# Performance work log

Hardware: AMD Instinct MI355X
Metric: run time of the kernel (lower is better)

Reference implementation:

```python
import jax, jax.numpy as jnp
import numpy as np

L_LAYERS = 2
N = 128
T = 64
K_BANDS = 30
KMOD = K_BANDS + 2  # 32
B = 4
G4 = 4 * N
EPS = 1e-5


def setup_inputs() -> dict:
    key = jax.random.key(0)
    ks = iter(jax.random.split(key, 32))
    s = 1.0 / np.sqrt(N)

    def u(shape):
        return jax.random.uniform(next(ks), shape, jnp.float32, -s, s)

    inp = {"x": jax.random.normal(next(ks), (B, KMOD, T, N), jnp.float32)}
    # temporal modules: KMOD LSTM/fc instances per layer
    inp["tw_ih"] = u((L_LAYERS, KMOD, 2, G4, N))
    inp["tw_hh"] = u((L_LAYERS, KMOD, 2, G4, N))
    inp["tb_ih"] = u((L_LAYERS, KMOD, 2, G4))
    inp["tb_hh"] = u((L_LAYERS, KMOD, 2, G4))
    inp["tfc_w"] = u((L_LAYERS, KMOD, N, 2 * N))
    inp["tfc_b"] = u((L_LAYERS, KMOD, N))
    inp["tgn_g"] = jnp.ones((L_LAYERS, N), jnp.float32)
    inp["tgn_b"] = jnp.zeros((L_LAYERS, N), jnp.float32)
    # band modules: T LSTM/fc instances per layer
    inp["bw_ih"] = u((L_LAYERS, T, 2, G4, N))
    inp["bw_hh"] = u((L_LAYERS, T, 2, G4, N))
    inp["bb_ih"] = u((L_LAYERS, T, 2, G4))
    inp["bb_hh"] = u((L_LAYERS, T, 2, G4))
    inp["bfc_w"] = u((L_LAYERS, T, N, 2 * N))
    inp["bfc_b"] = u((L_LAYERS, T, N))
    inp["bgn_g"] = jnp.ones((L_LAYERS, N), jnp.float32)
    inp["bgn_b"] = jnp.zeros((L_LAYERS, N), jnp.float32)
    return inp


def groupnorm(X, gamma, beta):
    # GroupNorm(1, N) on [B, N, K, T] == normalize over all non-batch dims,
    # per-channel affine on the last (N) dim of the [B, K, T, N] layout.
    mu = X.mean(axis=(1, 2, 3), keepdims=True)
    var = X.var(axis=(1, 2, 3), keepdims=True)
    return (X - mu) * jax.lax.rsqrt(var + EPS) * gamma + beta


def bilstm(x, w_ih, w_hh, b_ih, b_hh):
    # x: [B, S, N]; w_ih/w_hh: [2, 4N, N]; biases: [2, 4N]. PyTorch gate order i,f,g,o.
    Bb, S, n = x.shape

    def run(xs, wih, whh, b):
        pre = jnp.einsum('bsn,gn->bsg', xs, wih) + b  # [B, S, 4N]

        def step(carry, p):
            h, c = carry
            g = p + h @ whh.T
            i, f, gg, o = jnp.split(g, 4, axis=-1)
            c = jax.nn.sigmoid(f) * c + jax.nn.sigmoid(i) * jnp.tanh(gg)
            h = jax.nn.sigmoid(o) * jnp.tanh(c)
            return (h, c), h

        z = jnp.zeros((Bb, n), xs.dtype)
        _, hs = jax.lax.scan(step, (z, z), jnp.swapaxes(pre, 0, 1))
        return jnp.swapaxes(hs, 0, 1)  # [B, S, N]

    fwd = run(x, w_ih[0], w_hh[0], b_ih[0] + b_hh[0])
    bwd = run(x[:, ::-1], w_ih[1], w_hh[1], b_ih[1] + b_hh[1])[:, ::-1]
    return jnp.concatenate([fwd, bwd], axis=-1)  # [B, S, 2N]


# vmap over the per-instance (band or frame) leading axis of inputs and weights
vbilstm = jax.vmap(bilstm, in_axes=(0, 0, 0, 0, 0))


def temporal_module(X, w_ih, w_hh, b_ih, b_hh, fc_w, fc_b, g, b):
    skip = X  # [B, K, T, N]
    Xn = groupnorm(X, g, b)
    xs = jnp.swapaxes(Xn, 0, 1)  # [K, B, T, N]
    h = vbilstm(xs, w_ih, w_hh, b_ih, b_hh)  # [K, B, T, 2N]
    out = jnp.einsum('kbtd,knd->kbtn', h, fc_w) + fc_b[:, None, None, :]
    return jnp.swapaxes(out, 0, 1) + skip


def band_module(X, w_ih, w_hh, b_ih, b_hh, fc_w, fc_b, g, b):
    skip = X  # [B, K, T, N]
    Xn = groupnorm(X, g, b)
    xs = jnp.transpose(Xn, (2, 0, 1, 3))  # [T, B, K, N]
    h = vbilstm(xs, w_ih, w_hh, b_ih, b_hh)  # [T, B, K, 2N]
    out = jnp.einsum('tbkd,tnd->tbkn', h, fc_w) + fc_b[:, None, None, :]
    return jnp.transpose(out, (1, 2, 0, 3)) + skip


def reference(x, tw_ih, tw_hh, tb_ih, tb_hh, tfc_w, tfc_b, tgn_g, tgn_b,
              bw_ih, bw_hh, bb_ih, bb_hh, bfc_w, bfc_b, bgn_g, bgn_b):
    X = x
    for i in range(L_LAYERS):
        X = temporal_module(X, tw_ih[i], tw_hh[i], tb_ih[i], tb_hh[i],
                            tfc_w[i], tfc_b[i], tgn_g[i], tgn_b[i])
        X = band_module(X, bw_ih[i], bw_hh[i], bb_ih[i], bb_hh[i],
                        bfc_w[i], bfc_b[i], bgn_g[i], bgn_b[i])
    return X[:, :K_BANDS, :, :]
```

## Files before the change

### kernel.cpp

```cpp
#include <hip/hip_runtime.h>
#include <hip/hip_bf16.h>
#include <cstddef>

#define BB 4
#define KK 32
#define TTT 64
#define NNC 128
#define GG4 512

__global__ void k_copy(const float4* __restrict__ src, float4* __restrict__ dst, int n4) {
    int i = blockIdx.x * blockDim.x + threadIdx.x;
    if (i < n4) dst[i] = src[i];
}

__global__ void k_gnred(const float* __restrict__ X, float* __restrict__ red) {
    int b = blockIdx.x >> 6, chunk = blockIdx.x & 63;
    const float4* p4 = (const float4*)(X + (size_t)b * 262144 + (size_t)chunk * 4096);
    float s = 0.f, ss = 0.f;
#pragma unroll
    for (int i = 0; i < 4; ++i) {
        float4 v = p4[threadIdx.x + i * 256];
        s  += v.x + v.y + v.z + v.w;
        ss += v.x * v.x + v.y * v.y + v.z * v.z + v.w * v.w;
    }
    for (int off = 32; off; off >>= 1) {
        s  += __shfl_down(s, off);
        ss += __shfl_down(ss, off);
    }
    __shared__ float l0[4], l1[4];
    int w = threadIdx.x >> 6;
    if ((threadIdx.x & 63) == 0) { l0[w] = s; l1[w] = ss; }
    __syncthreads();
    if (threadIdx.x == 0) {
        float a = l0[0] + l0[1] + l0[2] + l0[3];
        float c = l1[0] + l1[1] + l1[2] + l1[3];
        red[(b * 64 + chunk) * 2]     = a;
        red[(b * 64 + chunk) * 2 + 1] = c;
    }
}

__device__ __forceinline__ float sigm(float x) { return 1.f / (1.f + __expf(-x)); }
__device__ __forceinline__ float tanh_fast(float x) {
    x = fminf(fmaxf(x, -15.f), 15.f);
    float e = __expf(2.f * x);
    return (e - 1.f) / (e + 1.f);
}

template <bool BAND>
__global__ __launch_bounds__(1024, 1) void k_pre(
    const float* __restrict__ X, float* __restrict__ pre,
    const float* __restrict__ red,
    const float* __restrict__ w_ih,
    const float* __restrict__ b_ih, const float* __restrict__ b_hh,
    const float* __restrict__ gn_g, const float* __restrict__ gn_b,
    int layer)
{
    constexpr int S    = BAND ? 32 : 64;
    constexpr int INST = BAND ? 64 : 32;
    const int tid = threadIdx.x;
    const int g   = tid & 511;
    const int hh  = tid >> 9;
    const int bid = blockIdx.x;
    const int b = bid & 3, dir = (bid >> 2) & 1, inst = bid >> 3;

    __shared__ float xn[S * 128];
    __shared__ float ex[4][1024];
    __shared__ float biasl[512];

    float s0 = 0.f, s1 = 0.f;
    {
        const float* rp = red + b * 128;
#pragma unroll 16
        for (int i = 0; i < 128; i += 2) { s0 += rp[i]; s1 += rp[i + 1]; }
    }
    const float mu = s0 * (1.0f / 262144.0f);
    const float rs = rsqrtf(fmaxf(s1 * (1.0f / 262144.0f) - mu * mu, 0.f) + 1e-5f);

    const size_t wbase = ((size_t)layer * INST + inst) * 2 + dir;
    if (tid < 512) biasl[tid] = b_ih[wbase * 512 + tid] + b_hh[wbase * 512 + tid];

    {
        const size_t xbase = BAND ? ((size_t)b * 2048 + inst) * 128
                                  : ((size_t)b * 32 + inst) * 64 * 128;
        const float* gmg = gn_g + layer * 128;
        const float* gmb = gn_b + layer * 128;
        for (int i4 = tid; i4 < S * 32; i4 += 1024) {
            int srow = i4 >> 5, n4 = i4 & 31;
            const float4 v = *(const float4*)(X + xbase +
                              (BAND ? (size_t)srow * 8192 : (size_t)srow * 128) + n4 * 4);
            const float4 ga = *(const float4*)(gmg + n4 * 4);
            const float4 be = *(const float4*)(gmb + n4 * 4);
            float4 o;
            o.x = (v.x - mu) * rs * ga.x + be.x;
            o.y = (v.y - mu) * rs * ga.y + be.y;
            o.z = (v.z - mu) * rs * ga.z + be.z;
            o.w = (v.w - mu) * rs * ga.w + be.w;
            *(float4*)(xn + srow * 128 + n4 * 4) = o;
        }
    }

    float4 w4[16];
    {
        const float* wr = w_ih + (wbase * 512 + g) * 128 + hh * 64;
#pragma unroll
        for (int j = 0; j < 16; ++j) w4[j] = *(const float4*)(wr + 4 * j);
    }
    __syncthreads();

    float* pb = pre + (size_t)bid * (S * 512);
    for (int st0 = 0; st0 < S; st0 += 4) {
#pragma unroll
        for (int q = 0; q < 4; ++q) {
            const int st = st0 + q;
            const int sidx = dir ? (S - 1 - st) : st;
            const float* xr = xn + sidx * 128 + hh * 64;
            float acc = 0.f;
#pragma unroll
            for (int j = 0; j < 16; ++j) {
                float4 hv = *(const float4*)(xr + 4 * j);
                acc += w4[j].x * hv.x + w4[j].y * hv.y + w4[j].z * hv.z + w4[j].w * hv.w;
            }
            ex[q][hh * 512 + g] = acc;
        }
        __syncthreads();
        for (int idx = tid; idx < 4 * 512; idx += 1024) {
            int q = idx >> 9, gg = idx & 511;
            pb[(size_t)(st0 + q) * 512 + gg] = ex[q][gg] + ex[q][512 + gg] + biasl[gg];
        }
        __syncthreads();
    }
}

template <bool BAND>
__global__ __launch_bounds__(1024, 1) void k_scan2(
    const float* __restrict__ pre, float* __restrict__ hout,
    const float* __restrict__ w_hh, int layer)
{
    constexpr int S    = BAND ? 32 : 64;
    constexpr int INST = BAND ? 64 : 32;
    constexpr int CH   = 8;
    const int tid = threadIdx.x;
    const int g   = tid & 511;
    const int hh  = tid >> 9;
    const int bid = blockIdx.x;
    const int b = bid & 3, dir = (bid >> 2) & 1, inst = bid >> 3;

    __shared__ float plds[2][CH * 512];
    __shared__ float ex[1024];
    __shared__ float hbuf[128];

    const size_t wbase = ((size_t)layer * INST + inst) * 2 + dir;
    float4 w4[16];
    {
        const float* wr = w_hh + (wbase * 512 + g) * 128 + hh * 64;
#pragma unroll
        for (int j = 0; j < 16; ++j) w4[j] = *(const float4*)(wr + 4 * j);
    }

    const float* pb = pre + (size_t)bid * (S * 512);
    ((float4*)plds[0])[tid] = ((const float4*)pb)[tid];
    if (tid < 128) hbuf[tid] = 0.f;
    float c = 0.f;
    float4 pf = make_float4(0.f, 0.f, 0.f, 0.f);
    __syncthreads();

    float* hob = hout + ((size_t)inst * 4 + b) * S * 256 + dir * 128;

    for (int ch = 0; ch < S / CH; ++ch) {
        const int buf = ch & 1;
        if (ch + 1 < S / CH)
            pf = ((const float4*)(pb + (size_t)(ch + 1) * CH * 512))[tid];
#pragma unroll
        for (int q = 0; q < CH; ++q) {
            const float* hr = hbuf + hh * 64;
            float acc = (hh == 0) ? plds[buf][q * 512 + g] : 0.f;
#pragma unroll
            for (int j = 0; j < 16; ++j) {
                float4 hv = *(const float4*)(hr + 4 * j);
                acc += w4[j].x * hv.x + w4[j].y * hv.y + w4[j].z * hv.z + w4[j].w * hv.w;
            }
            ex[hh * 512 + g] = acc;
            __syncthreads();
            if (tid < 128) {
                const float gi = ex[tid]       + ex[512 + tid];
                const float gf = ex[128 + tid] + ex[640 + tid];
                const float gg = ex[256 + tid] + ex[768 + tid];
                const float go = ex[384 + tid] + ex[896 + tid];
                c = sigm(gf) * c + sigm(gi) * tanh_fast(gg);
                const float hv = sigm(go) * tanh_fast(c);
                hbuf[tid] = hv;
                const int st = ch * CH + q;
                const int sidx = dir ? (S - 1 - st) : st;
                hob[(size_t)sidx * 256 + tid] = hv;
            }
            __syncthreads();
        }
        if (ch + 1 < S / CH) {
            ((float4*)plds[buf ^ 1])[tid] = pf;
            __syncthreads();
        }
    }
}

template <bool BAND>
__global__ void k_fc(const float* __restrict__ h, const float* __restrict__ fc_w,
                     const float* __restrict__ fc_b, float* __restrict__ X, int layer)
{
    constexpr int S    = BAND ? 32 : 64;
    constexpr int INST = BAND ? 64 : 32;
    constexpr int RPB  = 8;
    const int inst  = blockIdx.x / (BB * S / RPB);
    const int chunk = blockIdx.x % (BB * S / RPB);

    __shared__ float hs[RPB * 256];
    const int tid = threadIdx.x;
    const float* hbase = h + ((size_t)inst * BB * S + chunk * RPB) * 256;
    for (int i = tid; i < RPB * 64; i += 256)
        ((float4*)hs)[i] = ((const float4*)hbase)[i];
    __syncthreads();

    const int n  = tid & 127;
    const int rg = tid >> 7;
    const float* wrow = fc_w + (((size_t)layer * INST + inst) * 128 + n) * 256;
    float a0 = 0.f, a1 = 0.f, a2 = 0.f, a3 = 0.f;
#pragma unroll 8
    for (int d4 = 0; d4 < 64; ++d4) {
        float4 wv = ((const float4*)wrow)[d4];
        float4 h0 = ((const float4*)(hs + (rg * 4 + 0) * 256))[d4];
        float4 h1 = ((const float4*)(hs + (rg * 4 + 1) * 256))[d4];
        float4 h2 = ((const float4*)(hs + (rg * 4 + 2) * 256))[d4];
        float4 h3 = ((const float4*)(hs + (rg * 4 + 3) * 256))[d4];
        a0 += wv.x * h0.x + wv.y * h0.y + wv.z * h0.z + wv.w * h0.w;
        a1 += wv.x * h1.x + wv.y * h1.y + wv.z * h1.z + wv.w * h1.w;
        a2 += wv.x * h2.x + wv.y * h2.y + wv.z * h2.z + wv.w * h2.w;
        a3 += wv.x * h3.x + wv.y * h3.y + wv.z * h3.z + wv.w * h3.w;
    }
    const float bias = fc_b[((size_t)layer * INST + inst) * 128 + n];
    float acc[4] = {a0, a1, a2, a3};
#pragma unroll
    for (int i = 0; i < 4; ++i) {
        const int r = chunk * RPB + rg * 4 + i;
        const int b = r / S, s = r % S;
        const size_t xi = BAND ? (((size_t)b * 32 + s) * 64 + inst) * 128 + n
                               : (((size_t)b * 32 + inst) * 64 + s) * 128 + n;
        X[xi] += acc[i] + bias;
    }
}

__global__ void k_slice(const float* __restrict__ X, float* __restrict__ out) {
    int i = blockIdx.x * 256 + threadIdx.x;
    if (i >= 245760) return;
    int n4 = i & 31;
    int r  = i >> 5;
    int t  = r & 63;
    int bk = r >> 6;
    int k  = bk % 30, b = bk / 30;
    ((float4*)out)[i] = *(const float4*)(X + (((size_t)b * 32 + k) * 64 + t) * 128 + (size_t)n4 * 4);
}

extern "C" void kernel_launch(void* const* d_in, const int* in_sizes, int n_in,
                              void* d_out, int out_size, void* d_ws, size_t ws_size,
                              hipStream_t stream) {
    const float* x     = (const float*)d_in[0];
    const float* tw_ih = (const float*)d_in[1];
    const float* tw_hh = (const float*)d_in[2];
    const float* tb_ih = (const float*)d_in[3];
    const float* tb_hh = (const float*)d_in[4];
    const float* tfc_w = (const float*)d_in[5];
    const float* tfc_b = (const float*)d_in[6];
    const float* tgn_g = (const float*)d_in[7];
    const float* tgn_b = (const float*)d_in[8];
    const float* bw_ih = (const float*)d_in[9];
    const float* bw_hh = (const float*)d_in[10];
    const float* bb_ih = (const float*)d_in[11];
    const float* bb_hh = (const float*)d_in[12];
    const float* bfc_w = (const float*)d_in[13];
    const float* bfc_b = (const float*)d_in[14];
    const float* bgn_g = (const float*)d_in[15];
    const float* bgn_b = (const float*)d_in[16];

    float* X   = (float*)d_ws;
    float* h   = X + 1048576;
    float* red = h + 2097152;
    float* pre = red + 512;

    k_copy<<<1024, 256, 0, stream>>>((const float4*)x, (float4*)X, 262144);

    for (int layer = 0; layer < 2; ++layer) {
        k_gnred<<<256, 256, 0, stream>>>(X, red);
        k_pre<false><<<256, 1024, 0, stream>>>(X, pre, red, tw_ih, tb_ih, tb_hh,
                                               tgn_g, tgn_b, layer);
        k_scan2<false><<<256, 1024, 0, stream>>>(pre, h, tw_hh, layer);
        k_fc<false><<<1024, 256, 0, stream>>>(h, tfc_w, tfc_b, X, layer);
        k_gnred<<<256, 256, 0, stream>>>(X, red);
        k_pre<true><<<512, 1024, 0, stream>>>(X, pre, red, bw_ih, bb_ih, bb_hh,
                                              bgn_g, bgn_b, layer);
        k_scan2<true><<<512, 1024, 0, stream>>>(pre, h, bw_hh, layer);
        k_fc<true><<<1024, 256, 0, stream>>>(h, bfc_w, bfc_b, X, layer);
    }

    k_slice<<<960, 256, 0, stream>>>(X, (float*)d_out);
}
```

Before: 943.5 us.

## Fuse groupnorm stats into fc/copy, restructure LSTM scan with shuffle reductions

The standalone groupnorm reduction kernels are removed. Partial sum and sum-of-squares are now computed in the initial copy and in the epilogue of each fc kernel, and the final slice is written directly from the last band fc. The recurrent scan is reorganised so each hidden unit is handled by 8 lanes that own all four gates, reduced with xor shuffles. The pre-activations are stored gate-interleaved, and the h state is double-buffered, so each timestep needs one barrier instead of two. This cuts launches and per-step synchronisation, at the cost of more partial-sum reads in k_pre.

```diff
diff --git a/kernel.cpp b/kernel.cpp
--- a/kernel.cpp
+++ b/kernel.cpp
@@ -8,37 +8,6 @@
 #define NNC 128
 #define GG4 512
 
-__global__ void k_copy(const float4* __restrict__ src, float4* __restrict__ dst, int n4) {
-    int i = blockIdx.x * blockDim.x + threadIdx.x;
-    if (i < n4) dst[i] = src[i];
-}
-
-__global__ void k_gnred(const float* __restrict__ X, float* __restrict__ red) {
-    int b = blockIdx.x >> 6, chunk = blockIdx.x & 63;
-    const float4* p4 = (const float4*)(X + (size_t)b * 262144 + (size_t)chunk * 4096);
-    float s = 0.f, ss = 0.f;
-#pragma unroll
-    for (int i = 0; i < 4; ++i) {
-        float4 v = p4[threadIdx.x + i * 256];
-        s  += v.x + v.y + v.z + v.w;
-        ss += v.x * v.x + v.y * v.y + v.z * v.z + v.w * v.w;
-    }
-    for (int off = 32; off; off >>= 1) {
-        s  += __shfl_down(s, off);
-        ss += __shfl_down(ss, off);
-    }
-    __shared__ float l0[4], l1[4];
-    int w = threadIdx.x >> 6;
-    if ((threadIdx.x & 63) == 0) { l0[w] = s; l1[w] = ss; }
-    __syncthreads();
-    if (threadIdx.x == 0) {
-        float a = l0[0] + l0[1] + l0[2] + l0[3];
-        float c = l1[0] + l1[1] + l1[2] + l1[3];
-        red[(b * 64 + chunk) * 2]     = a;
-        red[(b * 64 + chunk) * 2 + 1] = c;
-    }
-}
-
 __device__ __forceinline__ float sigm(float x) { return 1.f / (1.f + __expf(-x)); }
 __device__ __forceinline__ float tanh_fast(float x) {
     x = fminf(fmaxf(x, -15.f), 15.f);
@@ -46,10 +15,32 @@
     return (e - 1.f) / (e + 1.f);
 }
 
+__global__ void k_copy_red(const float4* __restrict__ src, float4* __restrict__ dst,
+                           float* __restrict__ red2) {
+    const int i = blockIdx.x * 256 + threadIdx.x;
+    const float4 v = src[i];
+    dst[i] = v;
+    float s  = v.x + v.y + v.z + v.w;
+    float ss = v.x * v.x + v.y * v.y + v.z * v.z + v.w * v.w;
+    for (int off = 32; off; off >>= 1) {
+        s  += __shfl_down(s, off);
+        ss += __shfl_down(ss, off);
+    }
+    __shared__ float l0[4], l1[4];
+    const int w = threadIdx.x >> 6;
+    if ((threadIdx.x & 63) == 0) { l0[w] = s; l1[w] = ss; }
+    __syncthreads();
+    if (threadIdx.x == 0) {
+        const int b = blockIdx.x >> 8, slot = blockIdx.x & 255;
+        red2[(b * 256 + slot) * 2]     = l0[0] + l0[1] + l0[2] + l0[3];
+        red2[(b * 256 + slot) * 2 + 1] = l1[0] + l1[1] + l1[2] + l1[3];
+    }
+}
+
 template <bool BAND>
 __global__ __launch_bounds__(1024, 1) void k_pre(
     const float* __restrict__ X, float* __restrict__ pre,
-    const float* __restrict__ red,
+    const float* __restrict__ red2,
     const float* __restrict__ w_ih,
     const float* __restrict__ b_ih, const float* __restrict__ b_hh,
     const float* __restrict__ gn_g, const float* __restrict__ gn_b,
@@ -69,9 +60,9 @@
 
     float s0 = 0.f, s1 = 0.f;
     {
-        const float* rp = red + b * 128;
-#pragma unroll 16
-        for (int i = 0; i < 128; i += 2) { s0 += rp[i]; s1 += rp[i + 1]; }
+        const float* rp = red2 + b * 512;
+#pragma unroll 8
+        for (int i = 0; i < 512; i += 2) { s0 += rp[i]; s1 += rp[i + 1]; }
     }
     const float mu = s0 * (1.0f / 262144.0f);
     const float rs = rsqrtf(fmaxf(s1 * (1.0f / 262144.0f) - mu * mu, 0.f) + 1e-5f);
@@ -114,103 +105,147 @@
             const int st = st0 + q;
             const int sidx = dir ? (S - 1 - st) : st;
             const float* xr = xn + sidx * 128 + hh * 64;
-            float acc = 0.f;
-#pragma unroll
-            for (int j = 0; j < 16; ++j) {
-                float4 hv = *(const float4*)(xr + 4 * j);
-                acc += w4[j].x * hv.x + w4[j].y * hv.y + w4[j].z * hv.z + w4[j].w * hv.w;
+            float a0 = 0.f, a1 = 0.f, a2 = 0.f, a3 = 0.f;
+#pragma unroll
+            for (int j = 0; j < 4; ++j) {
+                float4 hv0 = *(const float4*)(xr + 16 * j);
+                float4 hv1 = *(const float4*)(xr + 16 * j + 4);
+                float4 hv2 = *(const float4*)(xr + 16 * j + 8);
+                float4 hv3 = *(const float4*)(xr + 16 * j + 12);
+                a0 += w4[4*j].x   * hv0.x + w4[4*j].y   * hv0.y + w4[4*j].z   * hv0.z + w4[4*j].w   * hv0.w;
+                a1 += w4[4*j+1].x * hv1.x + w4[4*j+1].y * hv1.y + w4[4*j+1].z * hv1.z + w4[4*j+1].w * hv1.w;
+                a2 += w4[4*j+2].x * hv2.x + w4[4*j+2].y * hv2.y + w4[4*j+2].z * hv2.z + w4[4*j+2].w * hv2.w;
+                a3 += w4[4*j+3].x * hv3.x + w4[4*j+3].y * hv3.y + w4[4*j+3].z * hv3.z + w4[4*j+3].w * hv3.w;
             }
-            ex[q][hh * 512 + g] = acc;
+            ex[q][hh * 512 + g] = (a0 + a1) + (a2 + a3);
         }
         __syncthreads();
         for (int idx = tid; idx < 4 * 512; idx += 1024) {
-            int q = idx >> 9, gg = idx & 511;
-            pb[(size_t)(st0 + q) * 512 + gg] = ex[q][gg] + ex[q][512 + gg] + biasl[gg];
+            const int q = idx >> 9, gg = idx & 511;
+            const int u = gg & 127, gt = gg >> 7;
+            pb[(size_t)(st0 + q) * 512 + u * 4 + gt] =
+                ex[q][gg] + ex[q][512 + gg] + biasl[gg];
         }
         __syncthreads();
     }
 }
 
 template <bool BAND>
-__global__ __launch_bounds__(1024, 1) void k_scan2(
+__global__ __launch_bounds__(1024, 1) void k_scan3(
     const float* __restrict__ pre, float* __restrict__ hout,
     const float* __restrict__ w_hh, int layer)
 {
     constexpr int S    = BAND ? 32 : 64;
     constexpr int INST = BAND ? 64 : 32;
     constexpr int CH   = 8;
+    constexpr int NCH  = S / CH;
     const int tid = threadIdx.x;
-    const int g   = tid & 511;
-    const int hh  = tid >> 9;
+    const int u   = tid >> 3;
+    const int j   = tid & 7;
     const int bid = blockIdx.x;
     const int b = bid & 3, dir = (bid >> 2) & 1, inst = bid >> 3;
 
     __shared__ float plds[2][CH * 512];
-    __shared__ float ex[1024];
-    __shared__ float hbuf[128];
+    __shared__ float hbuf[2][128];
 
     const size_t wbase = ((size_t)layer * INST + inst) * 2 + dir;
-    float4 w4[16];
+    float4 w4[4][4];
     {
-        const float* wr = w_hh + (wbase * 512 + g) * 128 + hh * 64;
-#pragma unroll
-        for (int j = 0; j < 16; ++j) w4[j] = *(const float4*)(wr + 4 * j);
+        const float* wb = w_hh + wbase * 512 * 128;
+#pragma unroll
+        for (int gt = 0; gt < 4; ++gt) {
+            const float* wr = wb + (size_t)(gt * 128 + u) * 128 + j * 16;
+#pragma unroll
+            for (int k = 0; k < 4; ++k) w4[gt][k] = *(const float4*)(wr + 4 * k);
+        }
     }
 
     const float* pb = pre + (size_t)bid * (S * 512);
     ((float4*)plds[0])[tid] = ((const float4*)pb)[tid];
-    if (tid < 128) hbuf[tid] = 0.f;
+    if (tid < 256) ((float*)hbuf)[tid] = 0.f;
+    __syncthreads();
+
     float c = 0.f;
-    float4 pf = make_float4(0.f, 0.f, 0.f, 0.f);
-    __syncthreads();
-
-    float* hob = hout + ((size_t)inst * 4 + b) * S * 256 + dir * 128;
-
-    for (int ch = 0; ch < S / CH; ++ch) {
+    float* hob = hout + (((size_t)inst * 4 + b) * S) * 256 + dir * 128;
+
+    int cur = 0;
+    float4 pf;
+    for (int ch = 0; ch < NCH; ++ch) {
         const int buf = ch & 1;
-        if (ch + 1 < S / CH)
+        if (ch + 1 < NCH)
             pf = ((const float4*)(pb + (size_t)(ch + 1) * CH * 512))[tid];
 #pragma unroll
         for (int q = 0; q < CH; ++q) {
-            const float* hr = hbuf + hh * 64;
-            float acc = (hh == 0) ? plds[buf][q * 512 + g] : 0.f;
-#pragma unroll
-            for (int j = 0; j < 16; ++j) {
-                float4 hv = *(const float4*)(hr + 4 * j);
-                acc += w4[j].x * hv.x + w4[j].y * hv.y + w4[j].z * hv.z + w4[j].w * hv.w;
+            const float* hr = &hbuf[cur][j * 16];
+            const float4 hv0 = *(const float4*)(hr);
+            const float4 hv1 = *(const float4*)(hr + 4);
+            const float4 hv2 = *(const float4*)(hr + 8);
+            const float4 hv3 = *(const float4*)(hr + 12);
+            float acc0, acc1, acc2, acc3;
+            {
+                float a;
+                a  = w4[0][0].x*hv0.x + w4[0][0].y*hv0.y + w4[0][0].z*hv0.z + w4[0][0].w*hv0.w;
+                a += w4[0][1].x*hv1.x + w4[0][1].y*hv1.y + w4[0][1].z*hv1.z + w4[0][1].w*hv1.w;
+                a += w4[0][2].x*hv2.x + w4[0][2].y*hv2.y + w4[0][2].z*hv2.z + w4[0][2].w*hv2.w;
+                a += w4[0][3].x*hv3.x + w4[0][3].y*hv3.y + w4[0][3].z*hv3.z + w4[0][3].w*hv3.w;
+                acc0 = a;
+                a  = w4[1][0].x*hv0.x + w4[1][0].y*hv0.y + w4[1][0].z*hv0.z + w4[1][0].w*hv0.w;
+                a += w4[1][1].x*hv1.x + w4[1][1].y*hv1.y + w4[1][1].z*hv1.z + w4[1][1].w*hv1.w;
+                a += w4[1][2].x*hv2.x + w4[1][2].y*hv2.y + w4[1][2].z*hv2.z + w4[1][2].w*hv2.w;
+                a += w4[1][3].x*hv3.x + w4[1][3].y*hv3.y + w4[1][3].z*hv3.z + w4[1][3].w*hv3.w;
+                acc1 = a;
+                a  = w4[2][0].x*hv0.x + w4[2][0].y*hv0.y + w4[2][0].z*hv0.z + w4[2][0].w*hv0.w;
+                a += w4[2][1].x*hv1.x + w4[2][1].y*hv1.y + w4[2][1].z*hv1.z + w4[2][1].w*hv1.w;
+                a += w4[2][2].x*hv2.x + w4[2][2].y*hv2.y + w4[2][2].z*hv2.z + w4[2][2].w*hv2.w;
+                a += w4[2][3].x*hv3.x + w4[2][3].y*hv3.y + w4[2][3].z*hv3.z + w4[2][3].w*hv3.w;
+                acc2 = a;
+                a  = w4[3][0].x*hv0.x + w4[3][0].y*hv0.y + w4[3][0].z*hv0.z + w4[3][0].w*hv0.w;
+                a += w4[3][1].x*hv1.x + w4[3][1].y*hv1.y + w4[3][1].z*hv1.z + w4[3][1].w*hv1.w;
+                a += w4[3][2].x*hv2.x + w4[3][2].y*hv2.y + w4[3][2].z*hv2.z + w4[3][2].w*hv2.w;
+                a += w4[3][3].x*hv3.x + w4[3][3].y*hv3.y + w4[3][3].z*hv3.z + w4[3][3].w*hv3.w;
+                acc3 = a;
             }
-            ex[hh * 512 + g] = acc;
-            __syncthreads();
-            if (tid < 128) {
-                const float gi = ex[tid]       + ex[512 + tid];
-                const float gf = ex[128 + tid] + ex[640 + tid];
-                const float gg = ex[256 + tid] + ex[768 + tid];
-                const float go = ex[384 + tid] + ex[896 + tid];
-                c = sigm(gf) * c + sigm(gi) * tanh_fast(gg);
-                const float hv = sigm(go) * tanh_fast(c);
-                hbuf[tid] = hv;
+#pragma unroll
+            for (int off = 1; off < 8; off <<= 1) {
+                acc0 += __shfl_xor(acc0, off);
+                acc1 += __shfl_xor(acc1, off);
+                acc2 += __shfl_xor(acc2, off);
+                acc3 += __shfl_xor(acc3, off);
+            }
+            const float4 p4 = *(const float4*)&plds[buf][q * 512 + u * 4];
+            const float gi = acc0 + p4.x;
+            const float gf = acc1 + p4.y;
+            const float gG = acc2 + p4.z;
+            const float go = acc3 + p4.w;
+            c = sigm(gf) * c + sigm(gi) * tanh_fast(gG);
+            const float hval = sigm(go) * tanh_fast(c);
+            const int nxt = cur ^ 1;
+            if (j == 0) {
+                hbuf[nxt][u] = hval;
                 const int st = ch * CH + q;
                 const int sidx = dir ? (S - 1 - st) : st;
-                hob[(size_t)sidx * 256 + tid] = hv;
+                hob[(size_t)sidx * 256 + u] = hval;
             }
+            if (q == CH - 1 && ch + 1 < NCH)
+                ((float4*)plds[buf ^ 1])[tid] = pf;
             __syncthreads();
-        }
-        if (ch + 1 < S / CH) {
-            ((float4*)plds[buf ^ 1])[tid] = pf;
-            __syncthreads();
+            cur = nxt;
         }
     }
 }
 
 template <bool BAND>
 __global__ void k_fc(const float* __restrict__ h, const float* __restrict__ fc_w,
-                     const float* __restrict__ fc_b, float* __restrict__ X, int layer)
+                     const float* __restrict__ fc_b, float* __restrict__ X,
+                     float* __restrict__ red2, float* __restrict__ out,
+                     int layer, int final_out)
 {
     constexpr int S    = BAND ? 32 : 64;
     constexpr int INST = BAND ? 64 : 32;
     constexpr int RPB  = 8;
-    const int inst  = blockIdx.x / (BB * S / RPB);
-    const int chunk = blockIdx.x % (BB * S / RPB);
+    constexpr int CPB  = S / RPB;
+    const int inst  = blockIdx.x / (BB * CPB);
+    const int chunk = blockIdx.x % (BB * CPB);
 
     __shared__ float hs[RPB * 256];
     const int tid = threadIdx.x;
@@ -222,7 +257,7 @@
     const int n  = tid & 127;
     const int rg = tid >> 7;
     const float* wrow = fc_w + (((size_t)layer * INST + inst) * 128 + n) * 256;
-    float a0 = 0.f, a1 = 0.f, a2 = 0.f, a3 = 0.f;
+    float4 a0 = {0,0,0,0}, a1 = {0,0,0,0}, a2 = {0,0,0,0}, a3 = {0,0,0,0};
 #pragma unroll 8
     for (int d4 = 0; d4 < 64; ++d4) {
         float4 wv = ((const float4*)wrow)[d4];
@@ -230,32 +265,45 @@
         float4 h1 = ((const float4*)(hs + (rg * 4 + 1) * 256))[d4];
         float4 h2 = ((const float4*)(hs + (rg * 4 + 2) * 256))[d4];
         float4 h3 = ((const float4*)(hs + (rg * 4 + 3) * 256))[d4];
-        a0 += wv.x * h0.x + wv.y * h0.y + wv.z * h0.z + wv.w * h0.w;
-        a1 += wv.x * h1.x + wv.y * h1.y + wv.z * h1.z + wv.w * h1.w;
-        a2 += wv.x * h2.x + wv.y * h2.y + wv.z * h2.z + wv.w * h2.w;
-        a3 += wv.x * h3.x + wv.y * h3.y + wv.z * h3.z + wv.w * h3.w;
+        a0.x += wv.x*h0.x; a0.y += wv.y*h0.y; a0.z += wv.z*h0.z; a0.w += wv.w*h0.w;
+        a1.x += wv.x*h1.x; a1.y += wv.y*h1.y; a1.z += wv.z*h1.z; a1.w += wv.w*h1.w;
+        a2.x += wv.x*h2.x; a2.y += wv.y*h2.y; a2.z += wv.z*h2.z; a2.w += wv.w*h2.w;
+        a3.x += wv.x*h3.x; a3.y += wv.y*h3.y; a3.z += wv.z*h3.z; a3.w += wv.w*h3.w;
     }
     const float bias = fc_b[((size_t)layer * INST + inst) * 128 + n];
-    float acc[4] = {a0, a1, a2, a3};
+    float acc[4];
+    acc[0] = (a0.x + a0.y) + (a0.z + a0.w);
+    acc[1] = (a1.x + a1.y) + (a1.z + a1.w);
+    acc[2] = (a2.x + a2.y) + (a2.z + a2.w);
+    acc[3] = (a3.x + a3.y) + (a3.z + a3.w);
+
+    float s = 0.f, ss = 0.f;
 #pragma unroll
     for (int i = 0; i < 4; ++i) {
         const int r = chunk * RPB + rg * 4 + i;
-        const int b = r / S, s = r % S;
-        const size_t xi = BAND ? (((size_t)b * 32 + s) * 64 + inst) * 128 + n
-                               : (((size_t)b * 32 + inst) * 64 + s) * 128 + n;
-        X[xi] += acc[i] + bias;
-    }
-}
-
-__global__ void k_slice(const float* __restrict__ X, float* __restrict__ out) {
-    int i = blockIdx.x * 256 + threadIdx.x;
-    if (i >= 245760) return;
-    int n4 = i & 31;
-    int r  = i >> 5;
-    int t  = r & 63;
-    int bk = r >> 6;
-    int k  = bk % 30, b = bk / 30;
-    ((float4*)out)[i] = *(const float4*)(X + (((size_t)b * 32 + k) * 64 + t) * 128 + (size_t)n4 * 4);
+        const int b = r / S, sd = r % S;
+        const size_t xi = BAND ? (((size_t)b * 32 + sd) * 64 + inst) * 128 + n
+                               : (((size_t)b * 32 + inst) * 64 + sd) * 128 + n;
+        const float v = X[xi] + acc[i] + bias;
+        X[xi] = v;
+        s += v; ss += v * v;
+        if (BAND && final_out && sd < 30)
+            out[(((size_t)b * 30 + sd) * 64 + inst) * 128 + n] = v;
+    }
+    for (int off = 32; off; off >>= 1) {
+        s  += __shfl_down(s, off);
+        ss += __shfl_down(ss, off);
+    }
+    __shared__ float l0[4], l1[4];
+    const int w = tid >> 6;
+    if ((tid & 63) == 0) { l0[w] = s; l1[w] = ss; }
+    __syncthreads();
+    if (tid == 0) {
+        const int bsel = chunk / CPB;
+        const int slot = inst * CPB + (chunk % CPB);
+        red2[(bsel * 256 + slot) * 2]     = l0[0] + l0[1] + l0[2] + l0[3];
+        red2[(bsel * 256 + slot) * 2 + 1] = l1[0] + l1[1] + l1[2] + l1[3];
+    }
 }
 
 extern "C" void kernel_launch(void* const* d_in, const int* in_sizes, int n_in,
@@ -279,25 +327,23 @@
     const float* bgn_g = (const float*)d_in[15];
     const float* bgn_b = (const float*)d_in[16];
 
-    float* X   = (float*)d_ws;
-    float* h   = X + 1048576;
-    float* red = h + 2097152;
-    float* pre = red + 512;
-
-    k_copy<<<1024, 256, 0, stream>>>((const float4*)x, (float4*)X, 262144);
+    float* X    = (float*)d_ws;
+    float* h    = X + 1048576;
+    float* red2 = h + 2097152;
+    float* pre  = red2 + 2048;
+    float* out  = (float*)d_out;
+
+    k_copy_red<<<1024, 256, 0, stream>>>((const float4*)x, (float4*)X, red2);
 
     for (int layer = 0; layer < 2; ++layer) {
-        k_gnred<<<256, 256, 0, stream>>>(X, red);
-        k_pre<false><<<256, 1024, 0, stream>>>(X, pre, red, tw_ih, tb_ih, tb_hh,
+        k_pre<false><<<256, 1024, 0, stream>>>(X, pre, red2, tw_ih, tb_ih, tb_hh,
                                                tgn_g, tgn_b, layer);
-        k_scan2<false><<<256, 1024, 0, stream>>>(pre, h, tw_hh, layer);
-        k_fc<false><<<1024, 256, 0, stream>>>(h, tfc_w, tfc_b, X, layer);
-        k_gnred<<<256, 256, 0, stream>>>(X, red);
-        k_pre<true><<<512, 1024, 0, stream>>>(X, pre, red, bw_ih, bb_ih, bb_hh,
+        k_scan3<false><<<256, 1024, 0, stream>>>(pre, h, tw_hh, layer);
+        k_fc<false><<<1024, 256, 0, stream>>>(h, tfc_w, tfc_b, X, red2, out, layer, 0);
+        k_pre<true><<<512, 1024, 0, stream>>>(X, pre, red2, bw_ih, bb_ih, bb_hh,
                                               bgn_g, bgn_b, layer);
-        k_scan2<true><<<512, 1024, 0, stream>>>(pre, h, bw_hh, layer);
-        k_fc<true><<<1024, 256, 0, stream>>>(h, bfc_w, bfc_b, X, layer);
-    }
-
-    k_slice<<<960, 256, 0, stream>>>(X, (float*)d_out);
-}
+        k_scan3<true><<<512, 1024, 0, stream>>>(pre, h, bw_hh, layer);
+        k_fc<true><<<1024, 256, 0, stream>>>(h, bfc_w, bfc_b, X, red2, out,
+                                             layer, layer == 1 ? 1 : 0);
+    }
+}
```

Result: slower. 987.8 us (+4.7%).
